# Optimization experiments

Hardware: AMD Instinct MI355X
Metric: run time of the kernel (lower is better)

The kernel has to match this reference:

```python
import jax, jax.numpy as jnp
import numpy as np

C = 192  # in_channels
B, S, L = 4, 64, 512  # batch, spatial (patch pixels), seq_len (num patches)


def setup_inputs() -> dict:
    key = jax.random.key(0)
    ks = jax.random.split(key, 6)
    scale_in = 1.0 / np.sqrt(C)
    return {
        "query": jax.random.normal(ks[0], (B, C, S, L), jnp.float32),
        "key": jax.random.normal(ks[1], (B, C, S, L), jnp.float32),
        "value": jax.random.normal(ks[2], (B, C, S, L), jnp.float32),
        "in_proj_weight": jax.random.normal(ks[3], (1 + 2 * C, C, 1, 1), jnp.float32) * scale_in,
        "in_proj_bias": jnp.zeros((1 + 2 * C,), jnp.float32),
        "out_proj_weight": jax.random.normal(ks[4], (C, C, 1, 1), jnp.float32) * scale_in,
        "out_proj_bias": jnp.zeros((C,), jnp.float32),
    }


def reference(query, key, value, in_proj_weight, in_proj_bias, out_proj_weight, out_proj_bias):
    # Separable (linear) attention, MobileViTv2-style.
    c = query.shape[1]
    w = in_proj_weight[:, :, 0, 0]           # (1+2C, C)
    wq, wk, wv = w[:1], w[1:1 + c], w[1 + c:]
    bq, bk, bv = in_proj_bias[:1], in_proj_bias[1:1 + c], in_proj_bias[1 + c:]

    # 1x1 conv projections (pointwise GEMMs over channels)
    q = jnp.einsum('oc,bcsl->bosl', wq, query) + bq[None, :, None, None]   # (B,1,S,L)
    k = jnp.einsum('oc,bcsl->bosl', wk, key) + bk[None, :, None, None]     # (B,C,S,L)
    v = jnp.einsum('oc,bcsl->bosl', wv, value) + bv[None, :, None, None]   # (B,C,S,L)

    # Context scores: softmax over token axis (seq_len); dropout_p=0 (eval)
    context_scores = jax.nn.softmax(q, axis=-1)                            # (B,1,S,L)

    # Weighted context pooling over tokens -> global context per spatial pixel
    context = jnp.sum(k * context_scores, axis=-1, keepdims=True)          # (B,C,S,1)

    # Broadcast multiply with gated value
    out = jax.nn.relu(v) * context                                         # (B,C,S,L)

    # Out projection (1x1 conv)
    wo = out_proj_weight[:, :, 0, 0]
    out = jnp.einsum('oc,bcsl->bosl', wo, out) + out_proj_bias[None, :, None, None]
    return out
```

## Files before the change

### kernel.cpp

```cpp
#include <hip/hip_runtime.h>

#define B_ 4
#define C_ 192
#define S_ 64
#define L_ 512

typedef _Float16 h8 __attribute__((ext_vector_type(8)));
typedef _Float16 h4 __attribute__((ext_vector_type(4)));
typedef _Float16 h2 __attribute__((ext_vector_type(2)));
typedef float f4 __attribute__((ext_vector_type(4)));

__device__ __forceinline__ int swz_l(int l) { return ((l >> 2) ^ l) & 7; }

__global__ __launch_bounds__(512) void k_prep(
    const float* __restrict__ W, const float* __restrict__ Bi,
    const float* __restrict__ Wo, const float* __restrict__ Bo,
    _Float16* __restrict__ wvh, _Float16* __restrict__ woh,
    float* __restrict__ bvf, float* __restrict__ bof)
{
    int n = blockIdx.x * 512 + threadIdx.x;
    if (n < 36864)       wvh[n] = (_Float16)W[37056 + n];
    else if (n < 73728)  woh[n - 36864] = (_Float16)Wo[n - 36864];
    else if (n < 73920)  bvf[n - 73728] = Bi[1 + C_ + (n - 73728)];
    else if (n < 74112)  bof[n - 73920] = Bo[n - 73920];
}

__global__ __launch_bounds__(512) void k1_qsoft(
    const float* __restrict__ Q, const float* __restrict__ W,
    float* __restrict__ pbuf)
{
    __shared__ float sm_wq[C_];
    __shared__ float sm_red[8];
    __shared__ float sm_red2[8];

    const int t = threadIdx.x;
    const int b = blockIdx.x >> 6, s = blockIdx.x & 63;
    const int lane = t & 63, w = t >> 6;

    if (t < C_) sm_wq[t] = W[t];
    __syncthreads();

    const float* qp = Q + ((size_t)(b * C_) * S_ + s) * L_ + t;
    float a0 = 0.f, a1 = 0.f, a2 = 0.f, a3 = 0.f;
    for (int c = 0; c < C_; c += 4) {
        a0 += sm_wq[c + 0] * qp[(size_t)(c + 0) * (S_ * L_)];
        a1 += sm_wq[c + 1] * qp[(size_t)(c + 1) * (S_ * L_)];
        a2 += sm_wq[c + 2] * qp[(size_t)(c + 2) * (S_ * L_)];
        a3 += sm_wq[c + 3] * qp[(size_t)(c + 3) * (S_ * L_)];
    }
    float q = (a0 + a1) + (a2 + a3);

    float m = q;
#pragma unroll
    for (int off = 32; off >= 1; off >>= 1) m = fmaxf(m, __shfl_down(m, off));
    if (lane == 0) sm_red[w] = m;
    __syncthreads();
    float bm = sm_red[0];
#pragma unroll
    for (int i = 1; i < 8; ++i) bm = fmaxf(bm, sm_red[i]);
    float e = __expf(q - bm);
    float sum = e;
#pragma unroll
    for (int off = 32; off >= 1; off >>= 1) sum += __shfl_down(sum, off);
    if (lane == 0) sm_red2[w] = sum;
    __syncthreads();
    float tot = 0.f;
#pragma unroll
    for (int i = 0; i < 8; ++i) tot += sm_red2[i];

    pbuf[(size_t)blockIdx.x * 512 + t] = e / tot;
}

__global__ __launch_bounds__(256) void k2_kbar(
    const float* __restrict__ K, const float* __restrict__ pbuf,
    float* __restrict__ kbar)
{
    const int t = threadIdx.x;
    const int bs = blockIdx.x / 6;
    const int cg = blockIdx.x - bs * 6;
    const int b = bs >> 6, s = bs & 63;
    const int wv = t >> 6, lane = t & 63;

    const f4* pp = (const f4*)(pbuf + (size_t)bs * 512);
    f4 p0 = pp[lane], p1 = pp[lane + 64];

    for (int r = 0; r < 8; ++r) {
        int c = cg * 32 + wv * 8 + r;
        const f4* kp = (const f4*)(K + ((size_t)(b * C_ + c) * S_ + s) * L_);
        f4 x0 = kp[lane], x1 = kp[lane + 64];
        float d = x0[0]*p0[0] + x0[1]*p0[1] + x0[2]*p0[2] + x0[3]*p0[3]
                + x1[0]*p1[0] + x1[1]*p1[1] + x1[2]*p1[2] + x1[3]*p1[3];
#pragma unroll
        for (int off = 32; off >= 1; off >>= 1) d += __shfl_down(d, off);
        if (lane == 0) kbar[(size_t)bs * C_ + c] = d;
    }
}

__global__ __launch_bounds__(192) void k3_ctx(
    const float* __restrict__ W, const float* __restrict__ Bi,
    const float* __restrict__ kbar, float* __restrict__ ctxb)
{
    __shared__ float kb[C_];
    const int t = threadIdx.x, bs = blockIdx.x;
    kb[t] = kbar[(size_t)bs * C_ + t];
    __syncthreads();
    const float* wr = W + (size_t)(1 + t) * C_;
    float a0 = 0.f, a1 = 0.f, a2 = 0.f, a3 = 0.f;
    for (int c = 0; c < C_; c += 4) {
        a0 += wr[c + 0] * kb[c + 0];
        a1 += wr[c + 1] * kb[c + 1];
        a2 += wr[c + 2] * kb[c + 2];
        a3 += wr[c + 3] * kb[c + 3];
    }
    ctxb[(size_t)bs * C_ + t] = (a0 + a1) + (a2 + a3) + Bi[1 + t];
}

__global__ __launch_bounds__(512, 4) void k_main(
    const float* __restrict__ V,
    const _Float16* __restrict__ wvh,
    const _Float16* __restrict__ woh,
    const float* __restrict__ ctxb,
    const float* __restrict__ bvf,
    const float* __restrict__ bof,
    float* __restrict__ Out)
{
    __shared__ __attribute__((aligned(16))) _Float16 sm_v[64 * 192];
    __shared__ __attribute__((aligned(16))) _Float16 sm_u[64 * 192];
    __shared__ __attribute__((aligned(16))) _Float16 sm_w[192 * 40];

    const int t = threadIdx.x;
    const int bs = blockIdx.x >> 3;
    const int chunk = blockIdx.x & 7;
    const int b = bs >> 6, s = bs & 63;
    const int l0 = chunk * 64;
    const int w = t >> 6, lane = t & 63;
    const int quad = lane >> 4, n16 = lane & 15;

    {
        const int tx = t & 15, rp = t >> 4;
        h2* smv2 = (h2*)sm_v;
#pragma unroll
        for (int i = 0; i < 3; ++i) {
            int cp = i * 32 + rp;
            const float* vp = V + ((size_t)(b * C_ + 2 * cp) * S_ + s) * L_ + l0 + tx * 4;
            f4 x0 = *(const f4*)vp;
            f4 x1 = *(const f4*)(vp + S_ * L_);
#pragma unroll
            for (int k = 0; k < 4; ++k) {
                int l = tx * 4 + k;
                int dw = l * 96 + (((cp >> 2) ^ swz_l(l)) << 2) + (cp & 3);
                h2 hh; hh[0] = (_Float16)x0[k]; hh[1] = (_Float16)x1[k];
                smv2[dw] = hh;
            }
        }
    }

    f4 acc[3][2];
#pragma unroll
    for (int i = 0; i < 3; ++i)
#pragma unroll
        for (int j = 0; j < 2; ++j) acc[i][j] = (f4)0.f;

    for (int kt = 0; kt < 6; ++kt) {
        __syncthreads();
        {
            const unsigned int* src = (const unsigned int*)wvh;
            unsigned int* dst = (unsigned int*)sm_w;
#pragma unroll
            for (int i = 0; i < 6; ++i) {
                int d = t + i * 512;
                int r = d >> 4, cd = d & 15;
                dst[r * 20 + cd] = src[r * 96 + kt * 16 + cd];
            }
        }
        __syncthreads();

        h8 bfr[2];
#pragma unroll
        for (int j = 0; j < 2; ++j) {
            int l = (w >> 2) * 32 + j * 16 + n16;
            bfr[j] = *(const h8*)(sm_v + l * 192 + ((((kt * 4 + quad)) ^ swz_l(l)) << 3));
        }
#pragma unroll
        for (int i = 0; i < 3; ++i) {
            int o = (w & 3) * 48 + i * 16 + n16;
            h8 afr = *(const h8*)(sm_w + o * 40 + quad * 8);
#pragma unroll
            for (int j = 0; j < 2; ++j)
                acc[i][j] = __builtin_amdgcn_mfma_f32_16x16x32_f16(afr, bfr[j], acc[i][j], 0, 0, 0);
        }
    }

#pragma unroll
    for (int i = 0; i < 3; ++i) {
        int o0 = (w & 3) * 48 + i * 16 + quad * 4;
        f4 cx = *(const f4*)(ctxb + (size_t)bs * C_ + o0);
        f4 bv = *(const f4*)(bvf + o0);
#pragma unroll
        for (int j = 0; j < 2; ++j) {
            int l = (w >> 2) * 32 + j * 16 + n16;
            h4 uu;
#pragma unroll
            for (int r = 0; r < 4; ++r) {
                float v = acc[i][j][r] + bv[r];
                uu[r] = (_Float16)(fmaxf(v, 0.f) * cx[r]);
            }
            *(h4*)(sm_u + l * 192 + (((o0 >> 3) ^ swz_l(l)) << 3) + (o0 & 7)) = uu;
        }
    }

    f4 acc2[2][3];
#pragma unroll
    for (int i = 0; i < 2; ++i)
#pragma unroll
        for (int j = 0; j < 3; ++j) acc2[i][j] = (f4)0.f;

    for (int kt = 0; kt < 6; ++kt) {
        __syncthreads();
        {
            const unsigned int* src = (const unsigned int*)woh;
            unsigned int* dst = (unsigned int*)sm_w;
#pragma unroll
            for (int i = 0; i < 6; ++i) {
                int d = t + i * 512;
                int r = d >> 4, cd = d & 15;
                dst[r * 20 + cd] = src[r * 96 + kt * 16 + cd];
            }
        }
        __syncthreads();

        h8 afr2[2];
#pragma unroll
        for (int i = 0; i < 2; ++i) {
            int l = (w >> 2) * 32 + i * 16 + n16;
            afr2[i] = *(const h8*)(sm_u + l * 192 + ((((kt * 4 + quad)) ^ swz_l(l)) << 3));
        }
#pragma unroll
        for (int j = 0; j < 3; ++j) {
            int p = (w & 3) * 48 + j * 16 + n16;
            h8 bfr = *(const h8*)(sm_w + p * 40 + quad * 8);
#pragma unroll
            for (int i = 0; i < 2; ++i)
                acc2[i][j] = __builtin_amdgcn_mfma_f32_16x16x32_f16(afr2[i], bfr, acc2[i][j], 0, 0, 0);
        }
    }

#pragma unroll
    for (int j = 0; j < 3; ++j) {
        int p = (w & 3) * 48 + j * 16 + n16;
        float bo = bof[p];
        float* obase = Out + ((size_t)(b * C_ + p) * S_ + s) * L_ + l0;
#pragma unroll
        for (int i = 0; i < 2; ++i) {
            int l = (w >> 2) * 32 + i * 16 + quad * 4;
            f4 ov = acc2[i][j];
            ov[0] += bo; ov[1] += bo; ov[2] += bo; ov[3] += bo;
            *(f4*)(obase + l) = ov;
        }
    }
}

extern "C" void kernel_launch(void* const* d_in, const int* in_sizes, int n_in,
                              void* d_out, int out_size, void* d_ws, size_t ws_size,
                              hipStream_t stream) {
    const float* Q  = (const float*)d_in[0];
    const float* K  = (const float*)d_in[1];
    const float* V  = (const float*)d_in[2];
    const float* W  = (const float*)d_in[3];
    const float* Bi = (const float*)d_in[4];
    const float* Wo = (const float*)d_in[5];
    const float* Bo = (const float*)d_in[6];
    float* Out = (float*)d_out;

    char* ws = (char*)d_ws;
    _Float16* wvh = (_Float16*)(ws);
    _Float16* woh = (_Float16*)(ws + 73728);
    float*    bvf = (float*)(ws + 147456);
    float*    bof = (float*)(ws + 148224);
    float*    pbuf = (float*)(ws + 148992);
    float*    kbar = (float*)(ws + 673280);
    float*    ctxb = (float*)(ws + 869888);

    k_prep  <<<dim3(145),      dim3(512), 0, stream>>>(W, Bi, Wo, Bo, wvh, woh, bvf, bof);
    k1_qsoft<<<dim3(B_ * S_),  dim3(512), 0, stream>>>(Q, W, pbuf);
    k2_kbar <<<dim3(B_*S_*6),  dim3(256), 0, stream>>>(K, pbuf, kbar);
    k3_ctx  <<<dim3(B_ * S_),  dim3(192), 0, stream>>>(W, Bi, kbar, ctxb);
    k_main  <<<dim3(B_*S_*8),  dim3(512), 0, stream>>>(V, wvh, woh, ctxb, bvf, bof, Out);
}
```

Baseline: 356.1 us.

## Fuse q-softmax, k pooling and context projection into one kernel; drop LDS weight staging

Merges the q projection and softmax, the weighted k pooling and the context projection into a single front kernel per (b,s). Intermediates now stay in shared memory, which removes two launches and the global round-trips for pbuf and kbar. The q projection now uses float4 loads split over four channel groups, and the key weight is pre-transposed in k_prep so reads are coalesced. In k_main, the per-kt shared-memory staging of fp16 weights and its barriers are replaced by direct global (L2-cached) fragment loads. The trade-off is only 256 front blocks with more serial work each, plus dependence on cache hits for the weight fragments.

```diff
diff --git a/kernel.cpp b/kernel.cpp
--- a/kernel.cpp
+++ b/kernel.cpp
@@ -16,20 +16,29 @@
     const float* __restrict__ W, const float* __restrict__ Bi,
     const float* __restrict__ Wo, const float* __restrict__ Bo,
     _Float16* __restrict__ wvh, _Float16* __restrict__ woh,
-    float* __restrict__ bvf, float* __restrict__ bof)
+    float* __restrict__ bvf, float* __restrict__ bof,
+    float* __restrict__ wkT)
 {
     int n = blockIdx.x * 512 + threadIdx.x;
     if (n < 36864)       wvh[n] = (_Float16)W[37056 + n];
     else if (n < 73728)  woh[n - 36864] = (_Float16)Wo[n - 36864];
     else if (n < 73920)  bvf[n - 73728] = Bi[1 + C_ + (n - 73728)];
     else if (n < 74112)  bof[n - 73920] = Bo[n - 73920];
-}
-
-__global__ __launch_bounds__(512) void k1_qsoft(
-    const float* __restrict__ Q, const float* __restrict__ W,
-    float* __restrict__ pbuf)
+    else if (n < 110976) {
+        int m = n - 74112;
+        int c = m / C_, o = m - c * C_;
+        wkT[m] = W[(1 + o) * C_ + c];
+    }
+}
+
+__global__ __launch_bounds__(512) void kA_front(
+    const float* __restrict__ Q, const float* __restrict__ K,
+    const float* __restrict__ W, const float* __restrict__ Bi,
+    const float* __restrict__ wkT, float* __restrict__ ctxb)
 {
-    __shared__ float sm_wq[C_];
+    __shared__ __attribute__((aligned(16))) float sm_part[4 * 512];
+    __shared__ float sm_p[512];
+    __shared__ float sm_kbar[C_];
     __shared__ float sm_red[8];
     __shared__ float sm_red2[8];
 
@@ -37,18 +46,22 @@
     const int b = blockIdx.x >> 6, s = blockIdx.x & 63;
     const int lane = t & 63, w = t >> 6;
 
-    if (t < C_) sm_wq[t] = W[t];
-    __syncthreads();
-
-    const float* qp = Q + ((size_t)(b * C_) * S_ + s) * L_ + t;
-    float a0 = 0.f, a1 = 0.f, a2 = 0.f, a3 = 0.f;
-    for (int c = 0; c < C_; c += 4) {
-        a0 += sm_wq[c + 0] * qp[(size_t)(c + 0) * (S_ * L_)];
-        a1 += sm_wq[c + 1] * qp[(size_t)(c + 1) * (S_ * L_)];
-        a2 += sm_wq[c + 2] * qp[(size_t)(c + 2) * (S_ * L_)];
-        a3 += sm_wq[c + 3] * qp[(size_t)(c + 3) * (S_ * L_)];
-    }
-    float q = (a0 + a1) + (a2 + a3);
+    {
+        const int qid = t & 127;
+        const int cg  = t >> 7;
+        const float* qp = Q + (((size_t)b * C_ + cg * 48) * S_ + s) * L_ + qid * 4;
+        f4 a; a[0] = 0.f; a[1] = 0.f; a[2] = 0.f; a[3] = 0.f;
+#pragma unroll 4
+        for (int c = 0; c < 48; ++c) {
+            float wq = W[cg * 48 + c];
+            f4 x = *(const f4*)(qp + (size_t)c * (S_ * L_));
+            a[0] += wq * x[0]; a[1] += wq * x[1]; a[2] += wq * x[2]; a[3] += wq * x[3];
+        }
+        *(f4*)&sm_part[cg * 512 + qid * 4] = a;
+    }
+    __syncthreads();
+
+    float q = (sm_part[t] + sm_part[512 + t]) + (sm_part[1024 + t] + sm_part[1536 + t]);
 
     float m = q;
 #pragma unroll
@@ -67,52 +80,36 @@
     float tot = 0.f;
 #pragma unroll
     for (int i = 0; i < 8; ++i) tot += sm_red2[i];
-
-    pbuf[(size_t)blockIdx.x * 512 + t] = e / tot;
-}
-
-__global__ __launch_bounds__(256) void k2_kbar(
-    const float* __restrict__ K, const float* __restrict__ pbuf,
-    float* __restrict__ kbar)
-{
-    const int t = threadIdx.x;
-    const int bs = blockIdx.x / 6;
-    const int cg = blockIdx.x - bs * 6;
-    const int b = bs >> 6, s = bs & 63;
-    const int wv = t >> 6, lane = t & 63;
-
-    const f4* pp = (const f4*)(pbuf + (size_t)bs * 512);
-    f4 p0 = pp[lane], p1 = pp[lane + 64];
-
-    for (int r = 0; r < 8; ++r) {
-        int c = cg * 32 + wv * 8 + r;
-        const f4* kp = (const f4*)(K + ((size_t)(b * C_ + c) * S_ + s) * L_);
-        f4 x0 = kp[lane], x1 = kp[lane + 64];
-        float d = x0[0]*p0[0] + x0[1]*p0[1] + x0[2]*p0[2] + x0[3]*p0[3]
-                + x1[0]*p1[0] + x1[1]*p1[1] + x1[2]*p1[2] + x1[3]*p1[3];
-#pragma unroll
-        for (int off = 32; off >= 1; off >>= 1) d += __shfl_down(d, off);
-        if (lane == 0) kbar[(size_t)bs * C_ + c] = d;
-    }
-}
-
-__global__ __launch_bounds__(192) void k3_ctx(
-    const float* __restrict__ W, const float* __restrict__ Bi,
-    const float* __restrict__ kbar, float* __restrict__ ctxb)
-{
-    __shared__ float kb[C_];
-    const int t = threadIdx.x, bs = blockIdx.x;
-    kb[t] = kbar[(size_t)bs * C_ + t];
-    __syncthreads();
-    const float* wr = W + (size_t)(1 + t) * C_;
-    float a0 = 0.f, a1 = 0.f, a2 = 0.f, a3 = 0.f;
-    for (int c = 0; c < C_; c += 4) {
-        a0 += wr[c + 0] * kb[c + 0];
-        a1 += wr[c + 1] * kb[c + 1];
-        a2 += wr[c + 2] * kb[c + 2];
-        a3 += wr[c + 3] * kb[c + 3];
-    }
-    ctxb[(size_t)bs * C_ + t] = (a0 + a1) + (a2 + a3) + Bi[1 + t];
+    sm_p[t] = e / tot;
+    __syncthreads();
+
+    {
+        const f4* pp = (const f4*)sm_p;
+        f4 p0 = pp[lane], p1 = pp[lane + 64];
+#pragma unroll 4
+        for (int r = 0; r < 24; ++r) {
+            int c = w * 24 + r;
+            const f4* kp = (const f4*)(K + (((size_t)b * C_ + c) * S_ + s) * L_);
+            f4 x0 = kp[lane], x1 = kp[lane + 64];
+            float d = x0[0]*p0[0] + x0[1]*p0[1] + x0[2]*p0[2] + x0[3]*p0[3]
+                    + x1[0]*p1[0] + x1[1]*p1[1] + x1[2]*p1[2] + x1[3]*p1[3];
+#pragma unroll
+            for (int off = 32; off >= 1; off >>= 1) d += __shfl_down(d, off);
+            if (lane == 0) sm_kbar[c] = d;
+        }
+    }
+    __syncthreads();
+
+    if (t < C_) {
+        float a0 = 0.f, a1 = 0.f, a2 = 0.f, a3 = 0.f;
+        for (int c = 0; c < C_; c += 4) {
+            a0 += wkT[(c + 0) * C_ + t] * sm_kbar[c + 0];
+            a1 += wkT[(c + 1) * C_ + t] * sm_kbar[c + 1];
+            a2 += wkT[(c + 2) * C_ + t] * sm_kbar[c + 2];
+            a3 += wkT[(c + 3) * C_ + t] * sm_kbar[c + 3];
+        }
+        ctxb[(size_t)blockIdx.x * C_ + t] = (a0 + a1) + (a2 + a3) + Bi[1 + t];
+    }
 }
 
 __global__ __launch_bounds__(512, 4) void k_main(
@@ -126,7 +123,6 @@
 {
     __shared__ __attribute__((aligned(16))) _Float16 sm_v[64 * 192];
     __shared__ __attribute__((aligned(16))) _Float16 sm_u[64 * 192];
-    __shared__ __attribute__((aligned(16))) _Float16 sm_w[192 * 40];
 
     const int t = threadIdx.x;
     const int bs = blockIdx.x >> 3;
@@ -154,6 +150,10 @@
             }
         }
     }
+    __syncthreads();
+
+    const int oB = (w & 3) * 48;
+    const int lB = (w >> 2) * 32;
 
     f4 acc[3][2];
 #pragma unroll
@@ -161,44 +161,33 @@
 #pragma unroll
         for (int j = 0; j < 2; ++j) acc[i][j] = (f4)0.f;
 
+#pragma unroll
     for (int kt = 0; kt < 6; ++kt) {
-        __syncthreads();
-        {
-            const unsigned int* src = (const unsigned int*)wvh;
-            unsigned int* dst = (unsigned int*)sm_w;
-#pragma unroll
-            for (int i = 0; i < 6; ++i) {
-                int d = t + i * 512;
-                int r = d >> 4, cd = d & 15;
-                dst[r * 20 + cd] = src[r * 96 + kt * 16 + cd];
-            }
-        }
-        __syncthreads();
-
+        h8 afr[3];
+#pragma unroll
+        for (int i = 0; i < 3; ++i)
+            afr[i] = *(const h8*)(wvh + (size_t)(oB + i * 16 + n16) * C_ + kt * 32 + quad * 8);
         h8 bfr[2];
 #pragma unroll
         for (int j = 0; j < 2; ++j) {
-            int l = (w >> 2) * 32 + j * 16 + n16;
-            bfr[j] = *(const h8*)(sm_v + l * 192 + ((((kt * 4 + quad)) ^ swz_l(l)) << 3));
-        }
-#pragma unroll
-        for (int i = 0; i < 3; ++i) {
-            int o = (w & 3) * 48 + i * 16 + n16;
-            h8 afr = *(const h8*)(sm_w + o * 40 + quad * 8);
+            int l = lB + j * 16 + n16;
+            bfr[j] = *(const h8*)(sm_v + l * 192 + (((kt * 4 + quad) ^ swz_l(l)) << 3));
+        }
+#pragma unroll
+        for (int i = 0; i < 3; ++i)
 #pragma unroll
             for (int j = 0; j < 2; ++j)
-                acc[i][j] = __builtin_amdgcn_mfma_f32_16x16x32_f16(afr, bfr[j], acc[i][j], 0, 0, 0);
-        }
+                acc[i][j] = __builtin_amdgcn_mfma_f32_16x16x32_f16(afr[i], bfr[j], acc[i][j], 0, 0, 0);
     }
 
 #pragma unroll
     for (int i = 0; i < 3; ++i) {
-        int o0 = (w & 3) * 48 + i * 16 + quad * 4;
+        int o0 = oB + i * 16 + quad * 4;
         f4 cx = *(const f4*)(ctxb + (size_t)bs * C_ + o0);
         f4 bv = *(const f4*)(bvf + o0);
 #pragma unroll
         for (int j = 0; j < 2; ++j) {
-            int l = (w >> 2) * 32 + j * 16 + n16;
+            int l = lB + j * 16 + n16;
             h4 uu;
 #pragma unroll
             for (int r = 0; r < 4; ++r) {
@@ -208,6 +197,7 @@
             *(h4*)(sm_u + l * 192 + (((o0 >> 3) ^ swz_l(l)) << 3) + (o0 & 7)) = uu;
         }
     }
+    __syncthreads();
 
     f4 acc2[2][3];
 #pragma unroll
@@ -215,44 +205,33 @@
 #pragma unroll
         for (int j = 0; j < 3; ++j) acc2[i][j] = (f4)0.f;
 
+#pragma unroll
     for (int kt = 0; kt < 6; ++kt) {
-        __syncthreads();
-        {
-            const unsigned int* src = (const unsigned int*)woh;
-            unsigned int* dst = (unsigned int*)sm_w;
-#pragma unroll
-            for (int i = 0; i < 6; ++i) {
-                int d = t + i * 512;
-                int r = d >> 4, cd = d & 15;
-                dst[r * 20 + cd] = src[r * 96 + kt * 16 + cd];
-            }
-        }
-        __syncthreads();
-
+        h8 bfr2[3];
+#pragma unroll
+        for (int j = 0; j < 3; ++j)
+            bfr2[j] = *(const h8*)(woh + (size_t)(oB + j * 16 + n16) * C_ + kt * 32 + quad * 8);
         h8 afr2[2];
 #pragma unroll
         for (int i = 0; i < 2; ++i) {
-            int l = (w >> 2) * 32 + i * 16 + n16;
-            afr2[i] = *(const h8*)(sm_u + l * 192 + ((((kt * 4 + quad)) ^ swz_l(l)) << 3));
-        }
-#pragma unroll
-        for (int j = 0; j < 3; ++j) {
-            int p = (w & 3) * 48 + j * 16 + n16;
-            h8 bfr = *(const h8*)(sm_w + p * 40 + quad * 8);
+            int l = lB + i * 16 + n16;
+            afr2[i] = *(const h8*)(sm_u + l * 192 + (((kt * 4 + quad) ^ swz_l(l)) << 3));
+        }
+#pragma unroll
+        for (int j = 0; j < 3; ++j)
 #pragma unroll
             for (int i = 0; i < 2; ++i)
-                acc2[i][j] = __builtin_amdgcn_mfma_f32_16x16x32_f16(afr2[i], bfr, acc2[i][j], 0, 0, 0);
-        }
+                acc2[i][j] = __builtin_amdgcn_mfma_f32_16x16x32_f16(afr2[i], bfr2[j], acc2[i][j], 0, 0, 0);
     }
 
 #pragma unroll
     for (int j = 0; j < 3; ++j) {
-        int p = (w & 3) * 48 + j * 16 + n16;
+        int p = oB + j * 16 + n16;
         float bo = bof[p];
         float* obase = Out + ((size_t)(b * C_ + p) * S_ + s) * L_ + l0;
 #pragma unroll
         for (int i = 0; i < 2; ++i) {
-            int l = (w >> 2) * 32 + i * 16 + quad * 4;
+            int l = lB + i * 16 + quad * 4;
             f4 ov = acc2[i][j];
             ov[0] += bo; ov[1] += bo; ov[2] += bo; ov[3] += bo;
             *(f4*)(obase + l) = ov;
@@ -277,13 +256,10 @@
     _Float16* woh = (_Float16*)(ws + 73728);
     float*    bvf = (float*)(ws + 147456);
     float*    bof = (float*)(ws + 148224);
-    float*    pbuf = (float*)(ws + 148992);
-    float*    kbar = (float*)(ws + 673280);
-    float*    ctxb = (float*)(ws + 869888);
-
-    k_prep  <<<dim3(145),      dim3(512), 0, stream>>>(W, Bi, Wo, Bo, wvh, woh, bvf, bof);
-    k1_qsoft<<<dim3(B_ * S_),  dim3(512), 0, stream>>>(Q, W, pbuf);
-    k2_kbar <<<dim3(B_*S_*6),  dim3(256), 0, stream>>>(K, pbuf, kbar);
-    k3_ctx  <<<dim3(B_ * S_),  dim3(192), 0, stream>>>(W, Bi, kbar, ctxb);
-    k_main  <<<dim3(B_*S_*8),  dim3(512), 0, stream>>>(V, wvh, woh, ctxb, bvf, bof, Out);
-}
+    float*    wkT = (float*)(ws + 148992);
+    float*    ctxb = (float*)(ws + 296448);
+
+    k_prep  <<<dim3(217),     dim3(512), 0, stream>>>(W, Bi, Wo, Bo, wvh, woh, bvf, bof, wkT);
+    kA_front<<<dim3(B_ * S_), dim3(512), 0, stream>>>(Q, K, W, Bi, wkT, ctxb);
+    k_main  <<<dim3(B_*S_*8), dim3(512), 0, stream>>>(V, wvh, woh, ctxb, bvf, bof, Out);
+}
```

After: 374.2 us. 1.05x slower.
